# Kernel tuning notes

Measured on AMD Instinct MI355X. Metric: run time of the kernel, lower is better.

## Reference

```python
import jax, jax.numpy as jnp
import numpy as np

SX = 4.0
SY = 4.0
H_DIM = 1024
B = 128
FH, FW = 24, 48


def setup_inputs() -> dict:
    key = jax.random.key(0)
    ks = jax.random.split(key, 8)
    s = lambda fan_in: 1.0 / np.sqrt(fan_in)
    return {
        "inp": jax.random.normal(ks[0], (B, H_DIM), jnp.float32),
        "hid": jax.random.normal(ks[1], (B, H_DIM), jnp.float32),
        "V": jax.random.normal(ks[2], (FH, FW, B, H_DIM), jnp.float32),
        "W1": jax.random.normal(ks[3], (2 * H_DIM, H_DIM), jnp.float32) * s(H_DIM),
        "b1": jnp.zeros((2 * H_DIM,), jnp.float32),
        "W2": jax.random.normal(ks[4], (2, 2 * H_DIM), jnp.float32) * s(2 * H_DIM),
        "b2": jnp.zeros((2,), jnp.float32),
        "Wc": jax.random.normal(ks[5], (H_DIM, 2 * H_DIM), jnp.float32) * s(2 * H_DIM),
        "bc": jnp.zeros((H_DIM,), jnp.float32),
    }


def reference(inp, hid, V, W1, b1, W2, b2, Wc, bc):
    h, w = V.shape[0], V.shape[1]
    # alignment MLP: Linear -> tanh -> Linear -> sigmoid, output [B, 2]
    algn = jax.nn.sigmoid(jnp.tanh(hid @ W1.T + b1) @ W2.T + b2)
    px, py = algn[:, 0], algn[:, 1]           # [B]
    x0 = (px * w)[:, None, None]              # [B,1,1]
    y0 = (py * h)[:, None, None]
    xs = jnp.arange(w, dtype=V.dtype)[None, None, :]   # [1,1,w]
    ys = jnp.arange(h, dtype=V.dtype)[None, :, None]   # [1,h,1]
    # Gaussian window weights over the feature map, [B,h,w]
    alpha = jnp.exp(-((xs - x0) ** 2 / (2.0 * SX * SX)
                      + (ys - y0) ** 2 / (2.0 * SY * SY)))
    alpha = alpha / alpha.sum(axis=(1, 2), keepdims=True)
    # weighted pooling over spatial dims: [B,h,w] x [h,w,B,H] -> [B,H]
    attn = jnp.einsum('brc,rcbh->bh', alpha, V)
    # contextualizer: Linear(2H, H) + ReLU on concat([inp, attn])
    ctx = jax.nn.relu(jnp.concatenate([inp, attn], axis=1) @ Wc.T + bc)
    return ctx
```

## Files before the change

kernel.cpp:

```cpp
#include <hip/hip_runtime.h>
#include <math.h>

#define NB 128
#define HD 1024
#define FHH 24
#define FWW 48

#define OFF_TPART 0u
#define OFF_X0    1048576u
#define OFF_Y0    1048704u
#define OFF_WXN   1048832u
#define OFF_WYN   1054976u
#define OFF_ATTN  1058048u

__global__ __launch_bounds__(256) void k_gemm1(
    const float* __restrict__ hid, const float* __restrict__ W1,
    float* __restrict__ tpart) {
  __shared__ float xs[128][36];
  __shared__ float wsh[32][36];
  const int tid = threadIdx.x;
  const int jt = blockIdx.x;
  const int ks = blockIdx.y;
  const int ty = tid >> 3, tx = tid & 7;
  const int b0 = ty * 4, jl = tx * 4;
  float acc[4][4] = {{0.f, 0.f, 0.f, 0.f}};
  for (int kt = 0; kt < 8; ++kt) {
    const int k0 = ks * 256 + kt * 32;
#pragma unroll
    for (int i = 0; i < 4; ++i) {
      int idx = tid + 256 * i;
      int bb = idx >> 3, q = idx & 7;
      float4 g = *(const float4*)(hid + bb * 1024 + k0 + q * 4);
      *(float4*)&xs[bb][q * 4] = g;
    }
    {
      int o = tid >> 3, q = tid & 7;
      float4 g = *(const float4*)(W1 + (size_t)(jt * 32 + o) * 1024 + k0 + q * 4);
      *(float4*)&wsh[o][q * 4] = g;
    }
    __syncthreads();
#pragma unroll
    for (int kk = 0; kk < 32; ++kk) {
      float xa[4], wb[4];
#pragma unroll
      for (int u = 0; u < 4; ++u) xa[u] = xs[b0 + u][kk];
#pragma unroll
      for (int v = 0; v < 4; ++v) wb[v] = wsh[jl + v][kk];
#pragma unroll
      for (int u = 0; u < 4; ++u)
#pragma unroll
        for (int v = 0; v < 4; ++v)
          acc[u][v] = fmaf(xa[u], wb[v], acc[u][v]);
    }
    __syncthreads();
  }
#pragma unroll
  for (int u = 0; u < 4; ++u)
#pragma unroll
    for (int v = 0; v < 4; ++v)
      tpart[(size_t)ks * (128u * 2048u) + (size_t)(b0 + u) * 2048u +
            (jt * 32 + jl + v)] = acc[u][v];
}

__global__ __launch_bounds__(256) void k_align(
    const float* __restrict__ tpart, const float* __restrict__ b1,
    const float* __restrict__ W2, const float* __restrict__ b2,
    float* __restrict__ x0a, float* __restrict__ y0a,
    float* __restrict__ wxn, float* __restrict__ wyn) {
  const int b = blockIdx.x;
  const int tid = threadIdx.x;
  float a0 = 0.f, a1 = 0.f;
#pragma unroll
  for (int i = 0; i < 8; ++i) {
    int j = tid + 256 * i;
    float s = b1[j];
    s += tpart[0u * 262144u + (size_t)b * 2048u + j];
    s += tpart[1u * 262144u + (size_t)b * 2048u + j];
    s += tpart[2u * 262144u + (size_t)b * 2048u + j];
    s += tpart[3u * 262144u + (size_t)b * 2048u + j];
    float tv = tanhf(s);
    a0 += tv * W2[j];
    a1 += tv * W2[2048 + j];
  }
  __shared__ float r0[256], r1[256];
  r0[tid] = a0; r1[tid] = a1;
  __syncthreads();
  for (int s = 128; s > 0; s >>= 1) {
    if (tid < s) { r0[tid] += r0[tid + s]; r1[tid] += r1[tid + s]; }
    __syncthreads();
  }
  __shared__ float xy[2];
  __shared__ float wxl[48], wyl[24];
  __shared__ float invZ[2];
  if (tid == 0) {
    float p0 = 1.f / (1.f + expf(-(r0[0] + b2[0])));
    float p1 = 1.f / (1.f + expf(-(r1[0] + b2[1])));
    xy[0] = p0 * 48.f;
    xy[1] = p1 * 24.f;
  }
  __syncthreads();
  float x0 = xy[0], y0 = xy[1];
  if (tid < 48) {
    float d = (float)tid - x0;
    wxl[tid] = expf(-d * d * (1.f / 32.f));
  } else if (tid >= 64 && tid < 88) {
    int r = tid - 64;
    float d = (float)r - y0;
    wyl[r] = expf(-d * d * (1.f / 32.f));
  }
  __syncthreads();
  if (tid == 0) {
    float zx = 0.f, zy = 0.f;
    for (int c = 0; c < 48; ++c) zx += wxl[c];
    for (int r = 0; r < 24; ++r) zy += wyl[r];
    invZ[0] = 1.f / zx;
    invZ[1] = 1.f / zy;
  }
  __syncthreads();
  if (tid < 48) wxn[b * 48 + tid] = wxl[tid] * invZ[0];
  else if (tid >= 64 && tid < 88) wyn[b * 24 + (tid - 64)] = wyl[tid - 64] * invZ[1];
  if (tid == 0) { x0a[b] = x0; y0a[b] = y0; }
}

__global__ __launch_bounds__(256) void k_attn(
    const float* __restrict__ V, const float* __restrict__ x0a,
    const float* __restrict__ y0a, const float* __restrict__ wxn,
    const float* __restrict__ wyn, float* __restrict__ attnp) {
  const int b = blockIdx.x;
  const int half = blockIdx.y;
  const int z = blockIdx.z;
  const int tid = threadIdx.x;
  __shared__ float wxl[48], wyl[24];
  __shared__ float xy[2];
  if (tid < 48) wxl[tid] = wxn[b * 48 + tid];
  else if (tid >= 64 && tid < 88) wyl[tid - 64] = wyn[b * 24 + (tid - 64)];
  if (tid == 96) xy[0] = x0a[b];
  if (tid == 97) xy[1] = y0a[b];
  __syncthreads();
  const float x0 = xy[0], y0 = xy[1];
  const int h0 = half * 512 + tid * 2;
  float accx = 0.f, accy = 0.f;
  const int r0 = max(0, (int)ceilf(y0 - 12.f));
  const int r1 = min(23, (int)floorf(y0 + 12.f));
  for (int r = r0 + z; r <= r1; r += 2) {
    float dy = (float)r - y0;
    float rem = 144.f - dy * dy;
    float rad = sqrtf(fmaxf(rem, 0.f));
    int c0 = max(0, (int)ceilf(x0 - rad));
    int c1 = min(47, (int)floorf(x0 + rad));
    float wy = wyl[r];
    for (int c = c0; c <= c1; ++c) {
      float w = wy * wxl[c];
      const float2 v =
          *(const float2*)(V + ((size_t)((r * 48 + c) * 128 + b)) * 1024u + h0);
      accx += w * v.x;
      accy += w * v.y;
    }
  }
  float2 o; o.x = accx; o.y = accy;
  *(float2*)(attnp + (size_t)z * 131072u + (size_t)b * 1024u + h0) = o;
}

__global__ __launch_bounds__(256) void k_gemm2(
    const float* __restrict__ inp, const float* __restrict__ attnp,
    const float* __restrict__ Wc, float* __restrict__ psum) {
  __shared__ float xs[128][36];
  __shared__ float wsh[32][36];
  const int tid = threadIdx.x;
  const int ot = blockIdx.x;
  const int ks = blockIdx.y;
  const int ty = tid >> 3, tx = tid & 7;
  const int b0 = ty * 4, ol = tx * 4;
  float acc[4][4] = {{0.f, 0.f, 0.f, 0.f}};
  for (int kt = 0; kt < 8; ++kt) {
    const int k0 = ks * 256 + kt * 32;
#pragma unroll
    for (int i = 0; i < 4; ++i) {
      int idx = tid + 256 * i;
      int bb = idx >> 3, q = idx & 7;
      float4 g;
      if (ks < 4) {
        g = *(const float4*)(inp + bb * 1024 + k0 + q * 4);
      } else {
        const float* p = attnp + bb * 1024 + (k0 - 1024) + q * 4;
        float4 ga = *(const float4*)p;
        float4 gb = *(const float4*)(p + 131072);
        g.x = ga.x + gb.x; g.y = ga.y + gb.y;
        g.z = ga.z + gb.z; g.w = ga.w + gb.w;
      }
      *(float4*)&xs[bb][q * 4] = g;
    }
    {
      int o = tid >> 3, q = tid & 7;
      float4 g = *(const float4*)(Wc + (size_t)(ot * 32 + o) * 2048u + k0 + q * 4);
      *(float4*)&wsh[o][q * 4] = g;
    }
    __syncthreads();
#pragma unroll
    for (int kk = 0; kk < 32; ++kk) {
      float xa[4], wb[4];
#pragma unroll
      for (int u = 0; u < 4; ++u) xa[u] = xs[b0 + u][kk];
#pragma unroll
      for (int v = 0; v < 4; ++v) wb[v] = wsh[ol + v][kk];
#pragma unroll
      for (int u = 0; u < 4; ++u)
#pragma unroll
        for (int v = 0; v < 4; ++v)
          acc[u][v] = fmaf(xa[u], wb[v], acc[u][v]);
    }
    __syncthreads();
  }
#pragma unroll
  for (int u = 0; u < 4; ++u)
#pragma unroll
    for (int v = 0; v < 4; ++v)
      psum[(size_t)ks * 131072u + (size_t)(b0 + u) * 1024u +
           (ot * 32 + ol + v)] = acc[u][v];
}

__global__ __launch_bounds__(256) void k_final(
    const float* __restrict__ psum, const float* __restrict__ bc,
    float* __restrict__ out) {
  const int gid = blockIdx.x * 256 + threadIdx.x;
  const int o = gid & 1023;
  float s = bc[o];
#pragma unroll
  for (int i = 0; i < 8; ++i) s += psum[(size_t)i * 131072u + gid];
  out[gid] = fmaxf(s, 0.f);
}

extern "C" void kernel_launch(void* const* d_in, const int* in_sizes, int n_in,
                              void* d_out, int out_size, void* d_ws,
                              size_t ws_size, hipStream_t stream) {
  const float* inp = (const float*)d_in[0];
  const float* hid = (const float*)d_in[1];
  const float* V   = (const float*)d_in[2];
  const float* W1  = (const float*)d_in[3];
  const float* b1  = (const float*)d_in[4];
  const float* W2  = (const float*)d_in[5];
  const float* b2  = (const float*)d_in[6];
  const float* Wc  = (const float*)d_in[7];
  const float* bc  = (const float*)d_in[8];
  float* out = (float*)d_out;
  float* ws = (float*)d_ws;

  float* tpart = ws + OFF_TPART;
  float* x0a   = ws + OFF_X0;
  float* y0a   = ws + OFF_Y0;
  float* wxn   = ws + OFF_WXN;
  float* wyn   = ws + OFF_WYN;
  float* attnp = ws + OFF_ATTN;

  k_gemm1<<<dim3(64, 4), 256, 0, stream>>>(hid, W1, tpart);
  k_align<<<128, 256, 0, stream>>>(tpart, b1, W2, b2, x0a, y0a, wxn, wyn);
  k_attn<<<dim3(128, 2, 2), 256, 0, stream>>>(V, x0a, y0a, wxn, wyn, attnp);
  k_gemm2<<<dim3(32, 8), 256, 0, stream>>>(inp, attnp, Wc, tpart);
  k_final<<<512, 256, 0, stream>>>(tpart, bc, out);
}
```

Baseline: 829.5 us.

## Restructure attention gather across row-warps and transpose GEMM smem tiles

The attention kernel now runs 512-thread blocks per batch row and quarter of H. Each of 8 warps takes a subset of spatial rows, loads V with float4 and reduces through shared memory, so the partial-attention buffer and its later summation go away. Both GEMMs store tiles k-major in shared memory so the inner loop reads float4 vectors instead of scalar strided loads, and they write outputs as float4. GEMM1 splits K eight ways for more blocks, which doubles the partial-sum buffer and moves the workspace offsets; in exchange the row loop in attention has uneven work across warps.

```diff
diff --git a/kernel.cpp b/kernel.cpp
--- a/kernel.cpp
+++ b/kernel.cpp
@@ -7,16 +7,16 @@
 #define FWW 48
 
 #define OFF_TPART 0u
-#define OFF_X0    1048576u
-#define OFF_Y0    1048704u
-#define OFF_WXN   1048832u
-#define OFF_WYN   1054976u
-#define OFF_ATTN  1058048u
+#define OFF_X0    2097152u
+#define OFF_Y0    2097280u
+#define OFF_WXN   2097408u
+#define OFF_WYN   2103552u
+#define OFF_ATTN  2106624u
 
 __global__ __launch_bounds__(256) void k_gemm1(
     const float* __restrict__ hid, const float* __restrict__ W1,
     float* __restrict__ tpart) {
-  __shared__ float xs[128][36];
+  __shared__ float xs[32][132];
   __shared__ float wsh[32][36];
   const int tid = threadIdx.x;
   const int jt = blockIdx.x;
@@ -24,42 +24,57 @@
   const int ty = tid >> 3, tx = tid & 7;
   const int b0 = ty * 4, jl = tx * 4;
   float acc[4][4] = {{0.f, 0.f, 0.f, 0.f}};
-  for (int kt = 0; kt < 8; ++kt) {
-    const int k0 = ks * 256 + kt * 32;
+  for (int kt = 0; kt < 4; ++kt) {
+    const int k0 = ks * 128 + kt * 32;
 #pragma unroll
     for (int i = 0; i < 4; ++i) {
       int idx = tid + 256 * i;
       int bb = idx >> 3, q = idx & 7;
       float4 g = *(const float4*)(hid + bb * 1024 + k0 + q * 4);
-      *(float4*)&xs[bb][q * 4] = g;
+      xs[q * 4 + 0][bb] = g.x;
+      xs[q * 4 + 1][bb] = g.y;
+      xs[q * 4 + 2][bb] = g.z;
+      xs[q * 4 + 3][bb] = g.w;
     }
     {
       int o = tid >> 3, q = tid & 7;
       float4 g = *(const float4*)(W1 + (size_t)(jt * 32 + o) * 1024 + k0 + q * 4);
-      *(float4*)&wsh[o][q * 4] = g;
+      wsh[q * 4 + 0][o] = g.x;
+      wsh[q * 4 + 1][o] = g.y;
+      wsh[q * 4 + 2][o] = g.z;
+      wsh[q * 4 + 3][o] = g.w;
     }
     __syncthreads();
 #pragma unroll
     for (int kk = 0; kk < 32; ++kk) {
-      float xa[4], wb[4];
-#pragma unroll
-      for (int u = 0; u < 4; ++u) xa[u] = xs[b0 + u][kk];
-#pragma unroll
-      for (int v = 0; v < 4; ++v) wb[v] = wsh[jl + v][kk];
-#pragma unroll
-      for (int u = 0; u < 4; ++u)
-#pragma unroll
-        for (int v = 0; v < 4; ++v)
-          acc[u][v] = fmaf(xa[u], wb[v], acc[u][v]);
-    }
-    __syncthreads();
-  }
-#pragma unroll
-  for (int u = 0; u < 4; ++u)
-#pragma unroll
-    for (int v = 0; v < 4; ++v)
-      tpart[(size_t)ks * (128u * 2048u) + (size_t)(b0 + u) * 2048u +
-            (jt * 32 + jl + v)] = acc[u][v];
+      float4 xa = *(const float4*)&xs[kk][b0];
+      float4 wb = *(const float4*)&wsh[kk][jl];
+      acc[0][0] = fmaf(xa.x, wb.x, acc[0][0]);
+      acc[0][1] = fmaf(xa.x, wb.y, acc[0][1]);
+      acc[0][2] = fmaf(xa.x, wb.z, acc[0][2]);
+      acc[0][3] = fmaf(xa.x, wb.w, acc[0][3]);
+      acc[1][0] = fmaf(xa.y, wb.x, acc[1][0]);
+      acc[1][1] = fmaf(xa.y, wb.y, acc[1][1]);
+      acc[1][2] = fmaf(xa.y, wb.z, acc[1][2]);
+      acc[1][3] = fmaf(xa.y, wb.w, acc[1][3]);
+      acc[2][0] = fmaf(xa.z, wb.x, acc[2][0]);
+      acc[2][1] = fmaf(xa.z, wb.y, acc[2][1]);
+      acc[2][2] = fmaf(xa.z, wb.z, acc[2][2]);
+      acc[2][3] = fmaf(xa.z, wb.w, acc[2][3]);
+      acc[3][0] = fmaf(xa.w, wb.x, acc[3][0]);
+      acc[3][1] = fmaf(xa.w, wb.y, acc[3][1]);
+      acc[3][2] = fmaf(xa.w, wb.z, acc[3][2]);
+      acc[3][3] = fmaf(xa.w, wb.w, acc[3][3]);
+    }
+    __syncthreads();
+  }
+#pragma unroll
+  for (int u = 0; u < 4; ++u) {
+    float4 o;
+    o.x = acc[u][0]; o.y = acc[u][1]; o.z = acc[u][2]; o.w = acc[u][3];
+    *(float4*)(tpart + (size_t)ks * 262144u + (size_t)(b0 + u) * 2048u +
+               (jt * 32 + jl)) = o;
+  }
 }
 
 __global__ __launch_bounds__(256) void k_align(
@@ -74,10 +89,9 @@
   for (int i = 0; i < 8; ++i) {
     int j = tid + 256 * i;
     float s = b1[j];
-    s += tpart[0u * 262144u + (size_t)b * 2048u + j];
-    s += tpart[1u * 262144u + (size_t)b * 2048u + j];
-    s += tpart[2u * 262144u + (size_t)b * 2048u + j];
-    s += tpart[3u * 262144u + (size_t)b * 2048u + j];
+#pragma unroll
+    for (int ks = 0; ks < 8; ++ks)
+      s += tpart[(size_t)ks * 262144u + (size_t)b * 2048u + j];
     float tv = tanhf(s);
     a0 += tv * W2[j];
     a1 += tv * W2[2048 + j];
@@ -122,101 +136,121 @@
   if (tid == 0) { x0a[b] = x0; y0a[b] = y0; }
 }
 
-__global__ __launch_bounds__(256) void k_attn(
+__global__ __launch_bounds__(512) void k_attn(
     const float* __restrict__ V, const float* __restrict__ x0a,
     const float* __restrict__ y0a, const float* __restrict__ wxn,
-    const float* __restrict__ wyn, float* __restrict__ attnp) {
+    const float* __restrict__ wyn, float* __restrict__ attn) {
   const int b = blockIdx.x;
-  const int half = blockIdx.y;
-  const int z = blockIdx.z;
-  const int tid = threadIdx.x;
+  const int qtr = blockIdx.y;
+  const int tid = threadIdx.x;
+  const int w = tid >> 6;
+  const int lane = tid & 63;
   __shared__ float wxl[48], wyl[24];
   __shared__ float xy[2];
+  __shared__ float red[8][260];
   if (tid < 48) wxl[tid] = wxn[b * 48 + tid];
   else if (tid >= 64 && tid < 88) wyl[tid - 64] = wyn[b * 24 + (tid - 64)];
   if (tid == 96) xy[0] = x0a[b];
   if (tid == 97) xy[1] = y0a[b];
   __syncthreads();
   const float x0 = xy[0], y0 = xy[1];
-  const int h0 = half * 512 + tid * 2;
-  float accx = 0.f, accy = 0.f;
-  const int r0 = max(0, (int)ceilf(y0 - 12.f));
-  const int r1 = min(23, (int)floorf(y0 + 12.f));
-  for (int r = r0 + z; r <= r1; r += 2) {
+  const int h0 = qtr * 256 + lane * 4;
+  float4 acc; acc.x = 0.f; acc.y = 0.f; acc.z = 0.f; acc.w = 0.f;
+  const int rlo = max(0, (int)ceilf(y0 - 12.f));
+  const int rhi = min(23, (int)floorf(y0 + 12.f));
+  for (int r = w; r < 24; r += 8) {
+    if (r < rlo || r > rhi) continue;
     float dy = (float)r - y0;
-    float rem = 144.f - dy * dy;
-    float rad = sqrtf(fmaxf(rem, 0.f));
+    float rad = sqrtf(fmaxf(144.f - dy * dy, 0.f));
     int c0 = max(0, (int)ceilf(x0 - rad));
     int c1 = min(47, (int)floorf(x0 + rad));
     float wy = wyl[r];
+    const float* base = V + ((size_t)((r * 48 + c0) * 128 + b)) * 1024u + h0;
+#pragma unroll 4
     for (int c = c0; c <= c1; ++c) {
-      float w = wy * wxl[c];
-      const float2 v =
-          *(const float2*)(V + ((size_t)((r * 48 + c) * 128 + b)) * 1024u + h0);
-      accx += w * v.x;
-      accy += w * v.y;
-    }
-  }
-  float2 o; o.x = accx; o.y = accy;
-  *(float2*)(attnp + (size_t)z * 131072u + (size_t)b * 1024u + h0) = o;
+      float wgt = wy * wxl[c];
+      const float4 v = *(const float4*)(base + (size_t)(c - c0) * 131072u);
+      acc.x = fmaf(wgt, v.x, acc.x);
+      acc.y = fmaf(wgt, v.y, acc.y);
+      acc.z = fmaf(wgt, v.z, acc.z);
+      acc.w = fmaf(wgt, v.w, acc.w);
+    }
+  }
+  *(float4*)&red[w][lane * 4] = acc;
+  __syncthreads();
+  if (tid < 256) {
+    float s = 0.f;
+#pragma unroll
+    for (int ww = 0; ww < 8; ++ww) s += red[ww][tid];
+    attn[(size_t)b * 1024u + qtr * 256 + tid] = s;
+  }
 }
 
 __global__ __launch_bounds__(256) void k_gemm2(
-    const float* __restrict__ inp, const float* __restrict__ attnp,
+    const float* __restrict__ inp, const float* __restrict__ attn,
     const float* __restrict__ Wc, float* __restrict__ psum) {
-  __shared__ float xs[128][36];
+  __shared__ float xs[32][132];
   __shared__ float wsh[32][36];
   const int tid = threadIdx.x;
   const int ot = blockIdx.x;
   const int ks = blockIdx.y;
   const int ty = tid >> 3, tx = tid & 7;
   const int b0 = ty * 4, ol = tx * 4;
+  const float* xsrc = (ks < 4) ? inp : attn;
+  const int kbase = (ks < 4) ? ks * 256 : (ks - 4) * 256;
   float acc[4][4] = {{0.f, 0.f, 0.f, 0.f}};
   for (int kt = 0; kt < 8; ++kt) {
-    const int k0 = ks * 256 + kt * 32;
+    const int k0g = ks * 256 + kt * 32;
+    const int k0x = kbase + kt * 32;
 #pragma unroll
     for (int i = 0; i < 4; ++i) {
       int idx = tid + 256 * i;
       int bb = idx >> 3, q = idx & 7;
-      float4 g;
-      if (ks < 4) {
-        g = *(const float4*)(inp + bb * 1024 + k0 + q * 4);
-      } else {
-        const float* p = attnp + bb * 1024 + (k0 - 1024) + q * 4;
-        float4 ga = *(const float4*)p;
-        float4 gb = *(const float4*)(p + 131072);
-        g.x = ga.x + gb.x; g.y = ga.y + gb.y;
-        g.z = ga.z + gb.z; g.w = ga.w + gb.w;
-      }
-      *(float4*)&xs[bb][q * 4] = g;
+      float4 g = *(const float4*)(xsrc + bb * 1024 + k0x + q * 4);
+      xs[q * 4 + 0][bb] = g.x;
+      xs[q * 4 + 1][bb] = g.y;
+      xs[q * 4 + 2][bb] = g.z;
+      xs[q * 4 + 3][bb] = g.w;
     }
     {
       int o = tid >> 3, q = tid & 7;
-      float4 g = *(const float4*)(Wc + (size_t)(ot * 32 + o) * 2048u + k0 + q * 4);
-      *(float4*)&wsh[o][q * 4] = g;
+      float4 g = *(const float4*)(Wc + (size_t)(ot * 32 + o) * 2048u + k0g + q * 4);
+      wsh[q * 4 + 0][o] = g.x;
+      wsh[q * 4 + 1][o] = g.y;
+      wsh[q * 4 + 2][o] = g.z;
+      wsh[q * 4 + 3][o] = g.w;
     }
     __syncthreads();
 #pragma unroll
     for (int kk = 0; kk < 32; ++kk) {
-      float xa[4], wb[4];
-#pragma unroll
-      for (int u = 0; u < 4; ++u) xa[u] = xs[b0 + u][kk];
-#pragma unroll
-      for (int v = 0; v < 4; ++v) wb[v] = wsh[ol + v][kk];
-#pragma unroll
-      for (int u = 0; u < 4; ++u)
-#pragma unroll
-        for (int v = 0; v < 4; ++v)
-          acc[u][v] = fmaf(xa[u], wb[v], acc[u][v]);
-    }
-    __syncthreads();
-  }
-#pragma unroll
-  for (int u = 0; u < 4; ++u)
-#pragma unroll
-    for (int v = 0; v < 4; ++v)
-      psum[(size_t)ks * 131072u + (size_t)(b0 + u) * 1024u +
-           (ot * 32 + ol + v)] = acc[u][v];
+      float4 xa = *(const float4*)&xs[kk][b0];
+      float4 wb = *(const float4*)&wsh[kk][ol];
+      acc[0][0] = fmaf(xa.x, wb.x, acc[0][0]);
+      acc[0][1] = fmaf(xa.x, wb.y, acc[0][1]);
+      acc[0][2] = fmaf(xa.x, wb.z, acc[0][2]);
+      acc[0][3] = fmaf(xa.x, wb.w, acc[0][3]);
+      acc[1][0] = fmaf(xa.y, wb.x, acc[1][0]);
+      acc[1][1] = fmaf(xa.y, wb.y, acc[1][1]);
+      acc[1][2] = fmaf(xa.y, wb.z, acc[1][2]);
+      acc[1][3] = fmaf(xa.y, wb.w, acc[1][3]);
+      acc[2][0] = fmaf(xa.z, wb.x, acc[2][0]);
+      acc[2][1] = fmaf(xa.z, wb.y, acc[2][1]);
+      acc[2][2] = fmaf(xa.z, wb.z, acc[2][2]);
+      acc[2][3] = fmaf(xa.z, wb.w, acc[2][3]);
+      acc[3][0] = fmaf(xa.w, wb.x, acc[3][0]);
+      acc[3][1] = fmaf(xa.w, wb.y, acc[3][1]);
+      acc[3][2] = fmaf(xa.w, wb.z, acc[3][2]);
+      acc[3][3] = fmaf(xa.w, wb.w, acc[3][3]);
+    }
+    __syncthreads();
+  }
+#pragma unroll
+  for (int u = 0; u < 4; ++u) {
+    float4 o;
+    o.x = acc[u][0]; o.y = acc[u][1]; o.z = acc[u][2]; o.w = acc[u][3];
+    *(float4*)(psum + (size_t)ks * 131072u + (size_t)(b0 + u) * 1024u +
+               (ot * 32 + ol)) = o;
+  }
 }
 
 __global__ __launch_bounds__(256) void k_final(
@@ -250,11 +284,11 @@
   float* y0a   = ws + OFF_Y0;
   float* wxn   = ws + OFF_WXN;
   float* wyn   = ws + OFF_WYN;
-  float* attnp = ws + OFF_ATTN;
-
-  k_gemm1<<<dim3(64, 4), 256, 0, stream>>>(hid, W1, tpart);
+  float* attn  = ws + OFF_ATTN;
+
+  k_gemm1<<<dim3(64, 8), 256, 0, stream>>>(hid, W1, tpart);
   k_align<<<128, 256, 0, stream>>>(tpart, b1, W2, b2, x0a, y0a, wxn, wyn);
-  k_attn<<<dim3(128, 2, 2), 256, 0, stream>>>(V, x0a, y0a, wxn, wyn, attnp);
-  k_gemm2<<<dim3(32, 8), 256, 0, stream>>>(inp, attnp, Wc, tpart);
+  k_attn<<<dim3(128, 4), 512, 0, stream>>>(V, x0a, y0a, wxn, wyn, attn);
+  k_gemm2<<<dim3(32, 8), 256, 0, stream>>>(inp, attn, Wc, tpart);
   k_final<<<512, 256, 0, stream>>>(tpart, bc, out);
 }
```

After: 743.1 us. 10.4% less time.
